# Performance work log

Measured on AMD Instinct MI355X. Metric: run time of the kernel, lower is better.

Reference implementation:

```python
import jax, jax.numpy as jnp
import numpy as np

B, D, L, K = 262144, 64, 4, 8
BOUND = 3.0
MIN_BW = 1e-3   # min bin width
MIN_BH = 1e-3   # min bin height
MIN_D = 1e-3    # min derivative
MIN_LAM = 0.025 # min lambda
EPS = 1e-6


def _knots(lengths, lo, hi):
    # lengths: (D, K) normalized bin fractions -> (bin lengths (D,K), knot positions (D,K+1))
    knots = jnp.cumsum(lengths, axis=-1)
    knots = jnp.pad(knots, ((0, 0), (1, 0)))
    knots = (hi - lo) * knots + lo
    knots = knots.at[..., 0].set(lo)
    knots = knots.at[..., -1].set(hi)
    return knots[..., 1:] - knots[..., :-1], knots


def _gather(p, idx):
    # p: (D, K'), idx: (B, D) -> (B, D): per-dimension bin-parameter gather
    return p[jnp.arange(p.shape[0])[None, :], idx]


def spline_layer(x, uw, uh, ud, ul):
    # x: (B, D); uw/uh/ul: (D, K); ud: (D, K-1). Linear-order monotonic rational spline (pyro).
    w = jax.nn.softmax(uw, axis=-1)
    h = jax.nn.softmax(uh, axis=-1)
    d = jax.nn.softplus(ud)
    lam = jax.nn.sigmoid(ul)

    num_bins = w.shape[-1]
    left, right = -BOUND, BOUND
    inside = (x >= left) & (x <= right)
    xc = jnp.clip(x, left, right)  # identity applied outside; clamp keeps inside-branch math finite

    w = MIN_BW + (1.0 - MIN_BW * num_bins) * w
    h = MIN_BH + (1.0 - MIN_BH * num_bins) * h
    d = MIN_D + d
    widths, cumw = _knots(w, left, right)
    heights, cumh = _knots(h, left, right)
    d = jnp.pad(d, ((0, 0), (1, 1)), constant_values=1.0)  # boundary derivatives fixed to 1
    lam = (1.0 - 2.0 * MIN_LAM) * lam + MIN_LAM

    # data-dependent bin search (searchsorted via comparison-sum, as in pyro)
    bin_idx = jnp.sum(xc[..., None] >= (cumw + EPS)[None], axis=-1) - 1  # (B, D)
    bin_idx = jnp.clip(bin_idx, 0, num_bins - 1)

    iw = _gather(widths, bin_idx)
    icw = _gather(cumw, bin_idx)
    ich = _gather(cumh, bin_idx)
    idelta = _gather(heights / widths, bin_idx)
    id0 = _gather(d[:, :-1], bin_idx)
    id1 = _gather(d[:, 1:], bin_idx)
    ih = _gather(heights, bin_idx)
    il = _gather(lam, bin_idx)

    wa = 1.0
    wb = jnp.sqrt(id0 / id1) * wa
    wc = (il * wa * id0 + (1.0 - il) * wb * id1) / idelta
    ya = ich
    yb = ih + ich
    yc = ((1.0 - il) * wa * ya + il * wb * yb) / ((1.0 - il) * wa + il * wb)

    theta = (xc - icw) / iw
    lower = theta <= il
    num = jnp.where(lower, wa * ya * (il - theta) + wc * yc * theta,
                    wc * yc * (1.0 - theta) + wb * yb * (theta - il))
    den = jnp.where(lower, wa * (il - theta) + wc * theta,
                    wc * (1.0 - theta) + wb * (theta - il))
    out = num / den
    dnum = jnp.where(lower, wa * wc * il * (yc - ya), wb * wc * (1.0 - il) * (yb - yc)) / iw
    lad = jnp.log(dnum) - 2.0 * jnp.log(jnp.abs(den))

    out = jnp.where(inside, out, x)
    lad = jnp.where(inside, lad, 0.0)
    return out, jnp.sum(lad, axis=1)


def setup_inputs() -> dict:
    key = jax.random.key(0)
    k0, k1, k2, k3, k4 = jax.random.split(key, 5)
    return {
        "x": jax.random.normal(k0, (B, D), dtype=jnp.float32),
        "uw": jax.random.normal(k1, (L, D, K), dtype=jnp.float32),
        "uh": jax.random.normal(k2, (L, D, K), dtype=jnp.float32),
        "ud": jax.random.normal(k3, (L, D, K - 1), dtype=jnp.float32),
        "ul": jax.random.uniform(k4, (L, D, K), dtype=jnp.float32),
    }


def reference(x, uw, uh, ud, ul):
    def step(carry, params):
        xi, ld = carry
        pw, ph, pd, pl = params
        xi, l = spline_layer(xi, pw, ph, pd, pl)
        return (xi, ld + l), None
    init = (x, jnp.zeros(x.shape[0], x.dtype))
    (x, log_det), _ = jax.lax.scan(step, init, (uw, uh, ud, ul))
    return x, log_det
```

## Files before the change

### kernel.cpp

```cpp
#include <hip/hip_runtime.h>


#define BATCH 262144
#define DIM   64
#define NLAY  4
#define NK    8

#define OFF_KN0 0
#define OFF_KN1 2048
#define OFF_CRS 4096
#define OFF_CF0 4544

__global__ void nf_pre(const float* __restrict__ uw, const float* __restrict__ uh,
                       const float* __restrict__ ud, const float* __restrict__ ul,
                       float* __restrict__ F) {
  __shared__ double Lb[NLAY][17], Ly[NLAY][17], LM[NLAY][16][4], Ld[NLAY][16];
  __shared__ double sx[64], Fb[65];
  int d = blockIdx.x;
  int t = threadIdx.x;

  if (t < 32) {
    int l = t >> 3, k = t & 7;
    const float* pw  = uw + (l*DIM + d)*NK;
    const float* ph  = uh + (l*DIM + d)*NK;
    const float* pdv = ud + (l*DIM + d)*(NK-1);
    const float* pl  = ul + (l*DIM + d)*NK;

    float ev[NK];
    float mw = pw[0];
    for (int j = 1; j < NK; ++j) mw = fmaxf(mw, pw[j]);
    float sw = 0.f;
    for (int j = 0; j < NK; ++j) { ev[j] = expf(pw[j] - mw); sw += ev[j]; }
    float invw = 1.f / sw;
    float cwe = 0.f, cwi = 0.f;
    for (int j = 0; j <= k; ++j) {
      float vj = 1e-3f + (1.f - 1e-3f * (float)NK) * (ev[j] * invw);
      cwe = cwi; cwi += vj;
    }
    float kwL = (k == 0) ? -3.f : 6.f * cwe - 3.f;
    float kwR = (k == 7) ?  3.f : 6.f * cwi - 3.f;
    float wwk = kwR - kwL;

    float mh = ph[0];
    for (int j = 1; j < NK; ++j) mh = fmaxf(mh, ph[j]);
    float sh = 0.f;
    for (int j = 0; j < NK; ++j) { ev[j] = expf(ph[j] - mh); sh += ev[j]; }
    float invh = 1.f / sh;
    float che = 0.f, chi = 0.f;
    for (int j = 0; j <= k; ++j) {
      float vj = 1e-3f + (1.f - 1e-3f * (float)NK) * (ev[j] * invh);
      che = chi; chi += vj;
    }
    float khL = (k == 0) ? -3.f : 6.f * che - 3.f;
    float khR = (k == 7) ?  3.f : 6.f * chi - 3.f;
    float hhk = khR - khL;

    float dvk, dvk1;
    if (k == 0) dvk = 1.f;
    else { float u = pdv[k-1]; dvk  = 1e-3f + (fmaxf(u,0.f) + log1pf(expf(-fabsf(u)))); }
    if (k == 7) dvk1 = 1.f;
    else { float u = pdv[k];   dvk1 = 1e-3f + (fmaxf(u,0.f) + log1pf(expf(-fabsf(u)))); }
    float sg = 1.f / (1.f + expf(-pl[k]));
    float lmk = 0.95f * sg + 0.025f;

    float delta = hhk / wwk;
    float wbf = sqrtf(dvk / dvk1);
    float wcf = (lmk*dvk + (1.f-lmk)*wbf*dvk1) / delta;
    float yaf = khL, ybf = hhk + khL;
    float ycf = ((1.f-lmk)*yaf + lmk*wbf*ybf) / ((1.f-lmk) + lmk*wbf);

    if (k == 0) {
      Lb[l][0] = -3.0; Lb[l][16] = 3.0;
      Ly[l][0] = -3.0; Ly[l][16] = 3.0;
    }
    if (k) Lb[l][2*k] = (double)(kwL + 1.0e-6f);
    Lb[l][2*k+1] = (double)kwL + (double)lmk*(double)wwk;
    Ly[l][2*k]   = (double)yaf;
    Ly[l][2*k+1] = (double)ycf;

    double icw = (double)kwL, iw = (double)wwk, il = (double)lmk;
    double wb = wbf, wc = wcf, ya = yaf, yb = ybf, yc = ycf;
    double n0 = ya*il, n1 = wc*yc - ya, d0 = il, d1 = wc - 1.0;
    double A = n1, Bv = n0*iw - n1*icw, C = d1, Dv = d0*iw - d1*icw;
    LM[l][2*k][0]=A; LM[l][2*k][1]=Bv; LM[l][2*k][2]=C; LM[l][2*k][3]=Dv;
    Ld[l][2*k] = log2(A*Dv - Bv*C);
    n0 = wc*yc - il*wb*yb; n1 = wb*yb - wc*yc; d0 = wc - il*wb; d1 = wb - wc;
    A = n1; Bv = n0*iw - n1*icw; C = d1; Dv = d0*iw - d1*icw;
    LM[l][2*k+1][0]=A; LM[l][2*k+1][1]=Bv; LM[l][2*k+1][2]=C; LM[l][2*k+1][3]=Dv;
    Ld[l][2*k+1] = log2(A*Dv - Bv*C);
  }
  __syncthreads();

  if (t < 60) {
    int lp  = t / 15;
    int mth = t % 15 + 1;
    double x = Lb[lp][mth];
    for (int q = lp - 1; q >= 0; --q) {
      int j = 0;
      for (int k = 1; k <= 15; ++k) j += (x >= Ly[q][k]) ? 1 : 0;
      const double* M = LM[q][j];
      x = (M[3]*x - M[1]) / (M[0] - M[2]*x);
    }
    sx[t] = x;
  }
  __syncthreads();
  if (t < 60) {
    double x = sx[t];
    int r = 0;
    for (int s2 = 0; s2 < 60; ++s2) {
      double o = sx[s2];
      r += (o < x || (o == x && s2 < t)) ? 1 : 0;
    }
    Fb[r+1] = x;
  }
  if (t == 0)  Fb[0] = -3.0;
  if (t >= 60) Fb[t+1] = 3.0;
  __syncthreads();

  {
    int j = t;
    float bf;
    if (j == 0)       bf = -3.0f;
    else if (j <= 60) bf = (float)Fb[j];
    else              bf = 1e30f;
    int cw = j >> 3, r8 = j & 7;
    if (r8 < 4) F[OFF_KN0 + (cw*DIM + d)*4 + r8]     = bf;
    else        F[OFF_KN1 + (cw*DIM + d)*4 + (r8-4)] = bf;
    if (j >= 8 && (j & 7) == 0 && j <= 56) F[OFF_CRS + (j/8 - 1)*DIM + d] = bf;
  }

  if (t < 61) {
    int p = t;
    double bl = Fb[p], br = Fb[p+1];
    float xmf = (float)(0.5*(bl+br));
    xmf = fminf(fmaxf(xmf, -3.f), 3.f);
    double y = (double)xmf;
    double A=1.0, Bv=0.0, C=0.0, Dv=1.0, ld2 = 0.0;
    for (int q = 0; q < NLAY; ++q) {
      int j = 0;
      for (int k = 1; k <= 15; ++k) j += (y >= Lb[q][k]) ? 1 : 0;
      const double* M = LM[q][j];
      ld2 += Ld[q][j];
      double A2 = M[0]*A + M[1]*C, B2 = M[0]*Bv + M[1]*Dv;
      double C2 = M[2]*A + M[3]*C, D2 = M[2]*Bv + M[3]*Dv;
      y = (M[0]*y + M[1]) / (M[2]*y + M[3]);
      A=A2; Bv=B2; C=C2; Dv=D2;
    }
    double sinv = exp2(-0.5 * ld2);
    float4 c4;
    c4.x = (float)(A*sinv); c4.y = (float)(Bv*sinv);
    c4.z = (float)(C*sinv); c4.w = (float)(Dv*sinv);
    *(float4*)(F + OFF_CF0 + (size_t)(p*DIM + d)*4) = c4;
  }
}

template <int CTRL>
__device__ __forceinline__ float dpp_add(float x) {
  int yi = __builtin_amdgcn_update_dpp(0, __float_as_int(x), CTRL, 0xF, 0xF, true);
  return x + __int_as_float(yi);
}
__device__ __forceinline__ float wave_sum63(float x) {
  x = dpp_add<0x111>(x);
  x = dpp_add<0x112>(x);
  x = dpp_add<0x114>(x);
  x = dpp_add<0x118>(x);
  x = dpp_add<0x142>(x);
  x = dpp_add<0x143>(x);
  return x;
}

__global__ __launch_bounds__(1024, 4) void nf_main(const float* __restrict__ X,
                                                   const float* __restrict__ F,
                                                   float* __restrict__ OUT,
                                                   float* __restrict__ LDo) {
  __shared__ float smem[19712];
  int t = threadIdx.x;
  {
    float4* dst = (float4*)smem;
    const float4* kt = (const float4*)(F + OFF_KN0);
    dst[t] = kt[t];
    const float4* ct = (const float4*)(F + OFF_CF0);
    for (int i = t; i < 3904; i += 1024) dst[1024 + i] = ct[i];
  }
  int d = t & 63;
  float k1 = F[OFF_CRS + 0*DIM + d];
  float k2 = F[OFF_CRS + 1*DIM + d];
  float k3 = F[OFF_CRS + 2*DIM + d];
  float k4 = F[OFF_CRS + 3*DIM + d];
  float k5 = F[OFF_CRS + 4*DIM + d];
  float k6 = F[OFF_CRS + 5*DIM + d];
  float k7 = F[OFF_CRS + 6*DIM + d];
  __syncthreads();
  const float4* skv = (const float4*)smem;

  int gw = blockIdx.x * 16 + (t >> 6);
  const float* Xp = X   + (size_t)gw*32*DIM + d;
  float*       Op = OUT + (size_t)gw*32*DIM + d;
  float*       Lp = LDo + (size_t)gw*32;

#define COARSE(xc) ((xc>=k1)+(xc>=k2)+(xc>=k3)+(xc>=k4)+(xc>=k5)+(xc>=k6)+(xc>=k7))
#define FINE(xc, cc, f0, f1) \
  ((cc<<3) + (int)(xc>=f0.y)+(int)(xc>=f0.z)+(int)(xc>=f0.w)+(int)(xc>=f1.x) \
           + (int)(xc>=f1.y)+(int)(xc>=f1.z)+(int)(xc>=f1.w))

  float xA0 = Xp[0], xA1 = Xp[64];
  float xB0 = Xp[128], xB1 = Xp[192];
  float xcA0 = __builtin_amdgcn_fmed3f(xA0, -3.f, 3.f);
  float xcA1 = __builtin_amdgcn_fmed3f(xA1, -3.f, 3.f);
  float4 cfA0, cfA1;
  {
    int c0 = COARSE(xcA0), c1 = COARSE(xcA1);
    float4 f00 = skv[(c0<<6)+d], f01 = skv[512+(c0<<6)+d];
    float4 f10 = skv[(c1<<6)+d], f11 = skv[512+(c1<<6)+d];
    int p0 = FINE(xcA0, c0, f00, f01);
    int p1 = FINE(xcA1, c1, f10, f11);
    cfA0 = skv[1024+(p0<<6)+d];
    cfA1 = skv[1024+(p1<<6)+d];
  }

  for (int g = 0; g < 3; ++g) {
#pragma unroll
    for (int u = 0; u < 5; ++u) {
      float xcB0 = __builtin_amdgcn_fmed3f(xB0, -3.f, 3.f);
      float xcB1 = __builtin_amdgcn_fmed3f(xB1, -3.f, 3.f);
      int cB0 = COARSE(xcB0), cB1 = COARSE(xcB1);
      float4 f00 = skv[(cB0<<6)+d], f01 = skv[512+(cB0<<6)+d];
      float4 f10 = skv[(cB1<<6)+d], f11 = skv[512+(cB1<<6)+d];
      int lo = (u == 4) ? ((g == 2) ? 5 : 6) : (u + 2);
      float xF0 = Xp[lo*128], xF1 = Xp[lo*128 + 64];
      __builtin_amdgcn_sched_barrier(0);
      float num0 = fmaf(cfA0.x, xcA0, cfA0.y);
      float den0 = fmaf(cfA0.z, xcA0, cfA0.w);
      float o0 = (xA0 == xcA0) ? __fdividef(num0, den0) : xA0;
      float l0 = __log2f(fabsf(den0));
      float num1 = fmaf(cfA1.x, xcA1, cfA1.y);
      float den1 = fmaf(cfA1.z, xcA1, cfA1.w);
      float o1 = (xA1 == xcA1) ? __fdividef(num1, den1) : xA1;
      float l1 = __log2f(fabsf(den1));
      Op[u*128] = o0; Op[u*128 + 64] = o1;
      float s0 = wave_sum63(l0);
      float s1 = wave_sum63(l1);
      if (d == 63) {
        float2 v;
        v.x = s0 * -1.3862943611198906f;
        v.y = s1 * -1.3862943611198906f;
        *(float2*)(Lp + 2*u) = v;
      }
      __builtin_amdgcn_sched_barrier(0);
      int p0 = FINE(xcB0, cB0, f00, f01);
      int p1 = FINE(xcB1, cB1, f10, f11);
      cfA0 = skv[1024+(p0<<6)+d];
      cfA1 = skv[1024+(p1<<6)+d];
      xA0 = xB0; xA1 = xB1; xcA0 = xcB0; xcA1 = xcB1;
      xB0 = xF0; xB1 = xF1;
    }
    Xp += 640; Op += 640; Lp += 10;
  }
  {
    float num0 = fmaf(cfA0.x, xcA0, cfA0.y);
    float den0 = fmaf(cfA0.z, xcA0, cfA0.w);
    float o0 = (xA0 == xcA0) ? __fdividef(num0, den0) : xA0;
    float l0 = __log2f(fabsf(den0));
    float num1 = fmaf(cfA1.x, xcA1, cfA1.y);
    float den1 = fmaf(cfA1.z, xcA1, cfA1.w);
    float o1 = (xA1 == xcA1) ? __fdividef(num1, den1) : xA1;
    float l1 = __log2f(fabsf(den1));
    Op[0] = o0; Op[64] = o1;
    float s0 = wave_sum63(l0);
    float s1 = wave_sum63(l1);
    if (d == 63) {
      float2 v;
      v.x = s0 * -1.3862943611198906f;
      v.y = s1 * -1.3862943611198906f;
      *(float2*)Lp = v;
    }
  }
#undef COARSE
#undef FINE
}

extern "C" void kernel_launch(void* const* d_in, const int* in_sizes, int n_in,
                              void* d_out, int out_size, void* d_ws, size_t ws_size,
                              hipStream_t stream) {
  const float* x  = (const float*)d_in[0];
  const float* uw = (const float*)d_in[1];
  const float* uh = (const float*)d_in[2];
  const float* ud = (const float*)d_in[3];
  const float* ul = (const float*)d_in[4];
  float* out = (float*)d_out;
  float* F = (float*)d_ws;
  nf_pre<<<DIM, 64, 0, stream>>>(uw, uh, ud, ul, F);
  nf_main<<<512, 1024, 0, stream>>>(x, F, out, out + (size_t)BATCH*DIM);
}
```

Baseline: 43.88 us.

## Store composed Möbius coefficients as fp16 recentered at piece left edge

The precompute kernel now recenters each piece's composed linear-fractional map at its left knot and stores the four coefficients as fp16 pairs (8 bytes instead of 16). This halves the coefficient table in shared memory. The main kernel replaces the 7-compare fine search with a 3-step branchless binary select that also yields the left knot, and blocks shrink from 1024 to 512 threads to raise occupancy. The fp16 coefficients add precision risk to the outputs and log-determinant.

```diff
diff --git a/kernel.cpp b/kernel.cpp
--- a/kernel.cpp
+++ b/kernel.cpp
@@ -1,4 +1,5 @@
 #include <hip/hip_runtime.h>
+#include <hip/hip_fp16.h>
 
 
 #define BATCH 262144
@@ -9,7 +10,7 @@
 #define OFF_KN0 0
 #define OFF_KN1 2048
 #define OFF_CRS 4096
-#define OFF_CF0 4544
+#define OFF_CFH 4544
 
 __global__ void nf_pre(const float* __restrict__ uw, const float* __restrict__ uh,
                        const float* __restrict__ ud, const float* __restrict__ ul,
@@ -146,11 +147,18 @@
       y = (M[0]*y + M[1]) / (M[2]*y + M[3]);
       A=A2; Bv=B2; C=C2; Dv=D2;
     }
+    float leftf = (p == 0) ? -3.0f : (float)bl;
+    double xl = (double)leftf;
+    double Bp = A*xl + Bv, Dp = C*xl + Dv;
     double sinv = exp2(-0.5 * ld2);
-    float4 c4;
-    c4.x = (float)(A*sinv); c4.y = (float)(Bv*sinv);
-    c4.z = (float)(C*sinv); c4.w = (float)(Dv*sinv);
-    *(float4*)(F + OFF_CF0 + (size_t)(p*DIM + d)*4) = c4;
+    float Af = (float)(A*sinv),  Bf = (float)(Bp*sinv);
+    float Cf = (float)(C*sinv),  Df = (float)(Dp*sinv);
+    __half2 hab = __floats2half2_rn(Af, Bf);
+    __half2 hcd = __floats2half2_rn(Cf, Df);
+    uint2 cw;
+    cw.x = __builtin_bit_cast(unsigned int, hab);
+    cw.y = __builtin_bit_cast(unsigned int, hcd);
+    *(uint2*)(F + OFF_CFH + (size_t)(p*DIM + d)*2) = cw;
   }
 }
 
@@ -169,18 +177,19 @@
   return x;
 }
 
-__global__ __launch_bounds__(1024, 4) void nf_main(const float* __restrict__ X,
-                                                   const float* __restrict__ F,
-                                                   float* __restrict__ OUT,
-                                                   float* __restrict__ LDo) {
-  __shared__ float smem[19712];
+__global__ __launch_bounds__(512, 6) void nf_main(const float* __restrict__ X,
+                                                  const float* __restrict__ F,
+                                                  float* __restrict__ OUT,
+                                                  float* __restrict__ LDo) {
+  __shared__ float smem[11904];
   int t = threadIdx.x;
   {
     float4* dst = (float4*)smem;
     const float4* kt = (const float4*)(F + OFF_KN0);
-    dst[t] = kt[t];
-    const float4* ct = (const float4*)(F + OFF_CF0);
-    for (int i = t; i < 3904; i += 1024) dst[1024 + i] = ct[i];
+    dst[t] = kt[t]; dst[t + 512] = kt[t + 512];
+    uint2* dh = (uint2*)(smem + 4096);
+    const uint2* ch = (const uint2*)(F + OFF_CFH);
+    for (int i = t; i < 3904; i += 512) dh[i] = ch[i];
   }
   int d = t & 63;
   float k1 = F[OFF_CRS + 0*DIM + d];
@@ -192,30 +201,46 @@
   float k7 = F[OFF_CRS + 6*DIM + d];
   __syncthreads();
   const float4* skv = (const float4*)smem;
-
-  int gw = blockIdx.x * 16 + (t >> 6);
+  const uint2*  scf = (const uint2*)(smem + 4096);
+
+  int gw = blockIdx.x * 8 + (t >> 6);
   const float* Xp = X   + (size_t)gw*32*DIM + d;
   float*       Op = OUT + (size_t)gw*32*DIM + d;
   float*       Lp = LDo + (size_t)gw*32;
 
 #define COARSE(xc) ((xc>=k1)+(xc>=k2)+(xc>=k3)+(xc>=k4)+(xc>=k5)+(xc>=k6)+(xc>=k7))
-#define FINE(xc, cc, f0, f1) \
-  ((cc<<3) + (int)(xc>=f0.y)+(int)(xc>=f0.z)+(int)(xc>=f0.w)+(int)(xc>=f1.x) \
-           + (int)(xc>=f1.y)+(int)(xc>=f1.z)+(int)(xc>=f1.w))
+#define FINEB(xc, cc, f0, f1, P, LF)                                          \
+  {                                                                           \
+    bool b4 = (xc) >= f1.x;                                                   \
+    float c2v = b4 ? f1.z : f0.z;                                             \
+    bool b2 = (xc) >= c2v;                                                    \
+    float c1a = b4 ? f1.y : f0.y;                                             \
+    float c1b = b4 ? f1.w : f0.w;                                             \
+    float c1v = b2 ? c1b : c1a;                                               \
+    bool b1 = (xc) >= c1v;                                                    \
+    float lf_ = f0.x;                                                         \
+    lf_ = b4 ? f1.x : lf_;                                                    \
+    lf_ = b2 ? c2v  : lf_;                                                    \
+    lf_ = b1 ? c1v  : lf_;                                                    \
+    P = ((cc)<<3) + (((int)b4)<<2) + (((int)b2)<<1) + (int)b1;                \
+    LF = lf_;                                                                 \
+  }
 
   float xA0 = Xp[0], xA1 = Xp[64];
   float xB0 = Xp[128], xB1 = Xp[192];
   float xcA0 = __builtin_amdgcn_fmed3f(xA0, -3.f, 3.f);
   float xcA1 = __builtin_amdgcn_fmed3f(xA1, -3.f, 3.f);
-  float4 cfA0, cfA1;
+  float lfA0, lfA1;
+  uint2 cwA0, cwA1;
   {
     int c0 = COARSE(xcA0), c1 = COARSE(xcA1);
     float4 f00 = skv[(c0<<6)+d], f01 = skv[512+(c0<<6)+d];
     float4 f10 = skv[(c1<<6)+d], f11 = skv[512+(c1<<6)+d];
-    int p0 = FINE(xcA0, c0, f00, f01);
-    int p1 = FINE(xcA1, c1, f10, f11);
-    cfA0 = skv[1024+(p0<<6)+d];
-    cfA1 = skv[1024+(p1<<6)+d];
+    int p0, p1;
+    FINEB(xcA0, c0, f00, f01, p0, lfA0)
+    FINEB(xcA1, c1, f10, f11, p1, lfA1)
+    cwA0 = scf[(p0<<6)+d];
+    cwA1 = scf[(p1<<6)+d];
   }
 
   for (int g = 0; g < 3; ++g) {
@@ -229,12 +254,18 @@
       int lo = (u == 4) ? ((g == 2) ? 5 : 6) : (u + 2);
       float xF0 = Xp[lo*128], xF1 = Xp[lo*128 + 64];
       __builtin_amdgcn_sched_barrier(0);
-      float num0 = fmaf(cfA0.x, xcA0, cfA0.y);
-      float den0 = fmaf(cfA0.z, xcA0, cfA0.w);
+      float2 ab0 = __half22float2(__builtin_bit_cast(__half2, cwA0.x));
+      float2 cd0 = __half22float2(__builtin_bit_cast(__half2, cwA0.y));
+      float2 ab1 = __half22float2(__builtin_bit_cast(__half2, cwA1.x));
+      float2 cd1 = __half22float2(__builtin_bit_cast(__half2, cwA1.y));
+      float t0 = xcA0 - lfA0;
+      float num0 = fmaf(ab0.x, t0, ab0.y);
+      float den0 = fmaf(cd0.x, t0, cd0.y);
       float o0 = (xA0 == xcA0) ? __fdividef(num0, den0) : xA0;
       float l0 = __log2f(fabsf(den0));
-      float num1 = fmaf(cfA1.x, xcA1, cfA1.y);
-      float den1 = fmaf(cfA1.z, xcA1, cfA1.w);
+      float t1 = xcA1 - lfA1;
+      float num1 = fmaf(ab1.x, t1, ab1.y);
+      float den1 = fmaf(cd1.x, t1, cd1.y);
       float o1 = (xA1 == xcA1) ? __fdividef(num1, den1) : xA1;
       float l1 = __log2f(fabsf(den1));
       Op[u*128] = o0; Op[u*128 + 64] = o1;
@@ -247,22 +278,31 @@
         *(float2*)(Lp + 2*u) = v;
       }
       __builtin_amdgcn_sched_barrier(0);
-      int p0 = FINE(xcB0, cB0, f00, f01);
-      int p1 = FINE(xcB1, cB1, f10, f11);
-      cfA0 = skv[1024+(p0<<6)+d];
-      cfA1 = skv[1024+(p1<<6)+d];
+      int p0, p1;
+      float lfN0, lfN1;
+      FINEB(xcB0, cB0, f00, f01, p0, lfN0)
+      FINEB(xcB1, cB1, f10, f11, p1, lfN1)
+      cwA0 = scf[(p0<<6)+d];
+      cwA1 = scf[(p1<<6)+d];
       xA0 = xB0; xA1 = xB1; xcA0 = xcB0; xcA1 = xcB1;
+      lfA0 = lfN0; lfA1 = lfN1;
       xB0 = xF0; xB1 = xF1;
     }
     Xp += 640; Op += 640; Lp += 10;
   }
   {
-    float num0 = fmaf(cfA0.x, xcA0, cfA0.y);
-    float den0 = fmaf(cfA0.z, xcA0, cfA0.w);
+    float2 ab0 = __half22float2(__builtin_bit_cast(__half2, cwA0.x));
+    float2 cd0 = __half22float2(__builtin_bit_cast(__half2, cwA0.y));
+    float2 ab1 = __half22float2(__builtin_bit_cast(__half2, cwA1.x));
+    float2 cd1 = __half22float2(__builtin_bit_cast(__half2, cwA1.y));
+    float t0 = xcA0 - lfA0;
+    float num0 = fmaf(ab0.x, t0, ab0.y);
+    float den0 = fmaf(cd0.x, t0, cd0.y);
     float o0 = (xA0 == xcA0) ? __fdividef(num0, den0) : xA0;
     float l0 = __log2f(fabsf(den0));
-    float num1 = fmaf(cfA1.x, xcA1, cfA1.y);
-    float den1 = fmaf(cfA1.z, xcA1, cfA1.w);
+    float t1 = xcA1 - lfA1;
+    float num1 = fmaf(ab1.x, t1, ab1.y);
+    float den1 = fmaf(cd1.x, t1, cd1.y);
     float o1 = (xA1 == xcA1) ? __fdividef(num1, den1) : xA1;
     float l1 = __log2f(fabsf(den1));
     Op[0] = o0; Op[64] = o1;
@@ -276,7 +316,7 @@
     }
   }
 #undef COARSE
-#undef FINE
+#undef FINEB
 }
 
 extern "C" void kernel_launch(void* const* d_in, const int* in_sizes, int n_in,
@@ -290,5 +330,5 @@
   float* out = (float*)d_out;
   float* F = (float*)d_ws;
   nf_pre<<<DIM, 64, 0, stream>>>(uw, uh, ud, ul, F);
-  nf_main<<<512, 1024, 0, stream>>>(x, F, out, out + (size_t)BATCH*DIM);
-}
+  nf_main<<<1024, 512, 0, stream>>>(x, F, out, out + (size_t)BATCH*DIM);
+}
```

Measured after the change: 45.96 us. 4.8% more time.
